# Performance work log

Measured on AMD Instinct MI355X. Metric: run time of the kernel, lower is better.

The kernel has to match this reference:

```python
import jax, jax.numpy as jnp
import numpy as np

B, S, D = 4, 2048, 1024

def setup_inputs() -> dict:
    key = jax.random.key(0)
    ks = jax.random.split(key, 7)
    sc = 1.0 / np.sqrt(D)
    return {
        "x": jax.random.normal(ks[0], (B, S, D), dtype=jnp.float32),
        "Wq": jax.random.normal(ks[1], (D, D), dtype=jnp.float32) * sc,
        "bq": jax.random.normal(ks[2], (D,), dtype=jnp.float32) * 0.01,
        "Wk": jax.random.normal(ks[3], (D, D), dtype=jnp.float32) * sc,
        "bk": jax.random.normal(ks[4], (D,), dtype=jnp.float32) * 0.01,
        "Wv": jax.random.normal(ks[5], (D, D), dtype=jnp.float32) * sc,
        "bv": jax.random.normal(ks[6], (D,), dtype=jnp.float32) * 0.01,
    }

def reference(x, Wq, bq, Wk, bk, Wv, bv):
    # q, k, v: [B, S, D] projections (torch Linear: x @ W^T + b; here W stored as [in, out])
    q = jnp.einsum("bsd,df->bsf", x, Wq) + bq
    k = jnp.einsum("bsd,df->bsf", x, Wk) + bk
    v = jnp.einsum("bsd,df->bsf", x, Wv) + bv
    dim = x.shape[-1]
    # scores: [B, S, S], scaled by sqrt(full d_model) as in the source
    scores = jnp.einsum("bqd,bkd->bqk", q, k) / jnp.sqrt(jnp.float32(dim)).astype(x.dtype)
    attn = jax.nn.softmax(scores, axis=-1)
    return jnp.einsum("bqk,bkd->bqd", attn, v)
```

## Files before the change

### kernel.cpp

```cpp
#include <hip/hip_runtime.h>
#include <hip/hip_bf16.h>

typedef __attribute__((ext_vector_type(8))) short bf16x8;
typedef __attribute__((ext_vector_type(4))) float f32x4;
typedef unsigned short u16;

__device__ __forceinline__ u16 f2bf(float f) {
  unsigned int u = __builtin_bit_cast(unsigned int, f);
  u += 0x7fffu + ((u >> 16) & 1u);
  return (u16)(u >> 16);
}
__device__ __forceinline__ float bf2f(unsigned int h) {
  unsigned int u = h << 16;
  return __builtin_bit_cast(float, u);
}

__device__ __forceinline__ void gload_lds16(const void* g, void* l) {
  __builtin_amdgcn_global_load_lds(
      (const __attribute__((address_space(1))) void*)g,
      (__attribute__((address_space(3))) void*)l, 16, 0, 0);
}

#define BAR() __builtin_amdgcn_s_barrier()
#define VMC(N) asm volatile("s_waitcnt vmcnt(%0)" ::"n"(N) : "memory")

template <int EPI>
__global__ __launch_bounds__(512, 2) void gemm8q(
    const u16* __restrict__ Abase, const u16* __restrict__ Btbase,
    const float* __restrict__ p0, float* __restrict__ p1,
    const float* __restrict__ p2, void* __restrict__ out0,
    void* __restrict__ out1, int Kd, int ldc, long long sAz, long long sBz,
    long long sCz) {
  constexpr int HSZ = 16384;
  constexpr int BUFSZ = 4 * HSZ;
  __shared__ char lds[2 * BUFSZ];

  const int gx = gridDim.x, gy = gridDim.y;
  const int nwg = gx * gy * gridDim.z;
  const int orig = blockIdx.x + gx * (blockIdx.y + gy * blockIdx.z);
  const int q = nwg >> 3, r = nwg & 7;
  const int xcd = orig & 7, loc = orig >> 3;
  const int wgid =
      (xcd < r ? xcd * (q + 1) : r * (q + 1) + (xcd - r) * q) + loc;
  const int bxi = wgid % gx;
  const int byi = (wgid / gx) % gy;
  const int z = wgid / (gx * gy);

  const int tid = threadIdx.x;
  const int w = tid >> 6, l = tid & 63;
  const int wr = w >> 2, wc = w & 3;
  const int lq = l >> 4, lr = l & 15;
  const int bm = byi * 256, bn = bxi * 256;
  const u16* A = Abase + (size_t)z * sAz;
  const u16* Bt = Btbase + (size_t)z * sBz;
  const int NT = Kd >> 6;

  const int kbp = ((tid & 7) ^ ((tid >> 3) & 7)) * 8;
  const int drow = tid >> 3;
  const u16* gA[2][2];
  const u16* gB[2][2];
#pragma unroll
  for (int h = 0; h < 2; ++h)
#pragma unroll
    for (int u = 0; u < 2; ++u) {
      gA[h][u] = A + (size_t)(bm + h * 128 + u * 64 + drow) * Kd + kbp;
      gB[h][u] = Bt + (size_t)(bn + h * 128 + u * 64 + drow) * Kd + kbp;
    }
  auto stageA = [&](int buf, int h, int kt) {
    char* d = lds + buf * BUFSZ + h * HSZ + tid * 16;
    gload_lds16(gA[h][0] + kt * 64, d);
    gload_lds16(gA[h][1] + kt * 64, d + 8192);
  };
  auto stageB = [&](int buf, int h, int kt) {
    char* d = lds + buf * BUFSZ + (2 + h) * HSZ + tid * 16;
    gload_lds16(gB[h][0] + kt * 64, d);
    gload_lds16(gB[h][1] + kt * 64, d + 8192);
  };

  const int ah = wr;
  const int bh = wc >> 1;
  const int bc0 = (wc & 1) * 64;
  const int sel = lr & 7;
  int koff[2];
#pragma unroll
  for (int kh = 0; kh < 2; ++kh) koff[kh] = (((kh * 4 + lq) ^ sel) << 4);

  f32x4 acc[8][4] = {};
  bf16x8 bb[4][2];
  bf16x8 a[2][2];

  stageA(0, 0, 0);
  stageA(0, 1, 0);
  stageB(0, 0, 0);
  stageB(0, 1, 0);
  stageA(1, 0, 1);
  stageA(1, 1, 1);
  stageB(1, 0, 1);
  stageB(1, 1, 1);
  VMC(8);
  BAR();

  for (int u = 0; u < NT; ++u) {
    const int buf = u & 1, obuf = buf ^ 1;
#pragma unroll
    for (int qp = 0; qp < 4; ++qp) {
      const char* pA = lds + buf * BUFSZ + ah * HSZ;
#pragma unroll
      for (int mf2 = 0; mf2 < 2; ++mf2)
#pragma unroll
        for (int kh = 0; kh < 2; ++kh)
          a[mf2][kh] = *(const bf16x8*)(pA + (qp * 32 + mf2 * 16 + lr) * 128 +
                                        koff[kh]);
      if (qp == 0) {
        const char* pB = lds + buf * BUFSZ + (2 + bh) * HSZ;
#pragma unroll
        for (int nf = 0; nf < 4; ++nf)
#pragma unroll
          for (int kh = 0; kh < 2; ++kh)
            bb[nf][kh] = *(const bf16x8*)(pB + (bc0 + nf * 16 + lr) * 128 +
                                          koff[kh]);
      }
      if (qp == 0 && u >= 1 && u + 1 < NT) stageA(obuf, 0, u + 1);
      if (qp == 1 && u >= 1 && u + 1 < NT) stageA(obuf, 1, u + 1);
      if (qp == 2 && u + 2 < NT) stageB(buf, 0, u + 2);
      if (qp == 3 && u + 2 < NT) stageB(buf, 1, u + 2);
      BAR();
      __builtin_amdgcn_s_setprio(1);
#pragma unroll
      for (int kh = 0; kh < 2; ++kh)
#pragma unroll
        for (int mf2 = 0; mf2 < 2; ++mf2)
#pragma unroll
          for (int nf = 0; nf < 4; ++nf)
            acc[qp * 2 + mf2][nf] = __builtin_amdgcn_mfma_f32_16x16x32_bf16(
                a[mf2][kh], bb[nf][kh], acc[qp * 2 + mf2][nf], 0, 0, 0);
      __builtin_amdgcn_s_setprio(0);
      if (qp == 3) {
        if (u + 2 < NT) {
          VMC(4);
        } else if (u + 1 < NT) {
          VMC(0);
        }
      }
      BAR();
    }
  }

  if constexpr (EPI == 4) {
    constexpr float K2 = 0.045084834f;
    u16* C = (u16*)out0 + (size_t)z * sCz;
    const float* cc = p0 + z * 2048;
    float* rs = p1 + z * 2048;
#pragma unroll
    for (int mf = 0; mf < 8; ++mf) {
      const int row = bm + wr * 128 + mf * 16 + lq * 4;
      float ps[4] = {0.f, 0.f, 0.f, 0.f};
#pragma unroll
      for (int nf = 0; nf < 4; ++nf) {
        const int col = bn + wc * 64 + nf * 16 + lr;
        const float cj2 = cc[col];
#pragma unroll
        for (int e = 0; e < 4; ++e) {
          const float pv = exp2f(fmaf(acc[mf][nf][e], K2, cj2));
          C[(size_t)(row + e) * ldc + col] = f2bf(pv);
          ps[e] += pv;
        }
      }
#pragma unroll
      for (int off = 1; off <= 8; off <<= 1)
#pragma unroll
        for (int e = 0; e < 4; ++e) ps[e] += __shfl_xor(ps[e], off, 64);
      if (lr == 0) {
#pragma unroll
        for (int e = 0; e < 4; ++e) atomicAdd(&rs[row + e], ps[e]);
      }
    }
  } else {
    const int mat = bn >> 10;
    u16* T = (u16*)out0;
    u16* V = (u16*)out1;
#pragma unroll
    for (int nf = 0; nf < 4; ++nf) {
      const int oc = (bn + wc * 64 + nf * 16 + lr) & 1023;
      if (mat == 0) {
#pragma unroll
        for (int mf = 0; mf < 8; ++mf) {
          const int row = bm + wr * 128 + mf * 16 + lq * 4;
#pragma unroll
          for (int e = 0; e < 4; ++e)
            T[(size_t)(row + e) * 1024 + oc] = f2bf(acc[mf][nf][e]);
        }
      } else {
        const float bb2 = p2[oc];
#pragma unroll
        for (int mf = 0; mf < 8; ++mf) {
          const int row = bm + wr * 128 + mf * 16 + lq * 4;
          const int bz = row >> 11, sdx = row & 2047;
          ushort4 pk;
          pk.x = f2bf(acc[mf][nf][0] + bb2);
          pk.y = f2bf(acc[mf][nf][1] + bb2);
          pk.z = f2bf(acc[mf][nf][2] + bb2);
          pk.w = f2bf(acc[mf][nf][3] + bb2);
          *(ushort4*)&V[((size_t)bz * 1024 + oc) * 2048 + sdx] = pk;
        }
      }
    }
  }
}

template <int EPI>
__global__ __launch_bounds__(512, 2) void gemm2t(
    const u16* __restrict__ Abase, const u16* __restrict__ Btbase,
    const float* __restrict__ p0, float* __restrict__ p1,
    const float* __restrict__ p2, void* __restrict__ out0,
    void* __restrict__ out1, int Kd, int ldc, long long sAz, long long sBz,
    long long sCz) {
  constexpr int ASZ = 16384;
  constexpr int BSZ = 32768;
  constexpr int BBASE = 2 * ASZ;
  __shared__ char lds[2 * ASZ + 3 * BSZ];

  const int gx = gridDim.x, gy = gridDim.y;
  const int nwg = gx * gy * gridDim.z;
  const int orig = blockIdx.x + gx * (blockIdx.y + gy * blockIdx.z);
  const int q = nwg >> 3, r = nwg & 7;
  const int xcd = orig & 7, loc = orig >> 3;
  const int wgid =
      (xcd < r ? xcd * (q + 1) : r * (q + 1) + (xcd - r) * q) + loc;
  const int bxi = wgid % gx;
  const int byi = (wgid / gx) % gy;
  const int z = wgid / (gx * gy);

  const int tid = threadIdx.x;
  const int w = tid >> 6, l = tid & 63;
  const int wr = w >> 2, wc = w & 3;
  const int lq = l >> 4, lr = l & 15;
  const int bm = byi * 128, bn = bxi * 256;
  const u16* A = Abase + (size_t)z * sAz;
  const u16* Bt = Btbase + (size_t)z * sBz;
  const int NT = Kd >> 6;

  const int kbp = ((tid & 7) ^ ((tid >> 3) & 7)) * 8;
  const int drow = tid >> 3;
  const u16* gA[2];
  const u16* gB[4];
#pragma unroll
  for (int u = 0; u < 2; ++u)
    gA[u] = A + (size_t)(bm + u * 64 + drow) * Kd + kbp;
#pragma unroll
  for (int u = 0; u < 4; ++u)
    gB[u] = Bt + (size_t)(bn + u * 64 + drow) * Kd + kbp;

  auto stageA = [&](int kt) {
    char* d = lds + (kt & 1) * ASZ + tid * 16;
#pragma unroll
    for (int u = 0; u < 2; ++u) gload_lds16(gA[u] + kt * 64, d + u * 8192);
  };
  auto stageB = [&](int kt) {
    char* d = lds + BBASE + (kt % 3) * BSZ + tid * 16;
#pragma unroll
    for (int u = 0; u < 4; ++u) gload_lds16(gB[u] + kt * 64, d + u * 8192);
  };

  const int rA = wr * 64 + lr;
  const int rB0 = wc * 64 + lr;
  int aoff[2];
#pragma unroll
  for (int kh = 0; kh < 2; ++kh)
    aoff[kh] = rA * 128 + (((kh * 4 + lq) ^ (rA & 7)) << 4);

  f32x4 acc[4][2][2] = {};
  bf16x8 a[2][4];
  bf16x8 bb[2][2][2];

  auto rdA = [&](int kt) {
    const char* p = lds + (kt & 1) * ASZ;
#pragma unroll
    for (int kh = 0; kh < 2; ++kh)
#pragma unroll
      for (int mf = 0; mf < 4; ++mf)
        a[kh][mf] = *(const bf16x8*)(p + aoff[kh] + mf * 2048);
  };
  auto rdB = [&](int kt) {
    const char* p = lds + BBASE + (kt % 3) * BSZ;
#pragma unroll
    for (int nh = 0; nh < 2; ++nh) {
      const int rB = rB0 + nh * 32;
#pragma unroll
      for (int kh = 0; kh < 2; ++kh) {
        const int o = rB * 128 + (((kh * 4 + lq) ^ (rB & 7)) << 4);
#pragma unroll
        for (int nf = 0; nf < 2; ++nf)
          bb[nh][kh][nf] = *(const bf16x8*)(p + o + nf * 2048);
      }
    }
  };
  auto mma = [&](int kh) {
    __builtin_amdgcn_s_setprio(1);
#pragma unroll
    for (int nh = 0; nh < 2; ++nh)
#pragma unroll
      for (int mf = 0; mf < 4; ++mf)
#pragma unroll
        for (int nf = 0; nf < 2; ++nf)
          acc[mf][nh][nf] = __builtin_amdgcn_mfma_f32_16x16x32_bf16(
              a[kh][mf], bb[nh][kh][nf], acc[mf][nh][nf], 0, 0, 0);
    __builtin_amdgcn_s_setprio(0);
  };

  stageB(0);
  stageA(0);
  stageB(1);
  stageA(1);
  VMC(6);
  BAR();

  for (int t = 0; t < NT; ++t) {
    rdA(t);
    rdB(t);
    if (t + 2 < NT) stageB(t + 2);
    BAR();
    mma(0);
    if (t + 2 < NT) VMC(4); else VMC(0);
    BAR();
    if (t + 2 < NT) stageA(t + 2);
    mma(1);
  }

  float* C = (float*)out0 + (size_t)z * sCz;
  const float* rs = p1 + z * 2048;
#pragma unroll
  for (int nh = 0; nh < 2; ++nh)
#pragma unroll
    for (int nf = 0; nf < 2; ++nf) {
      const int col = bn + wc * 64 + nh * 32 + nf * 16 + lr;
#pragma unroll
      for (int mf = 0; mf < 4; ++mf) {
        const int row = bm + wr * 64 + mf * 16 + lq * 4;
#pragma unroll
        for (int e = 0; e < 4; ++e)
          C[(size_t)(row + e) * ldc + col] = acc[mf][nh][nf][e] / rs[row + e];
      }
    }
}

__global__ __launch_bounds__(256) void gemmM(
    const u16* __restrict__ Abase, const u16* __restrict__ Btbase,
    float* __restrict__ out0, int Kd, int Kext, int ldc, long long sAz,
    long long sBz, long long sCz) {
  constexpr int ASZ = 16384;
  constexpr int BSZ = 16384;
  constexpr int BBASE = 2 * ASZ;
  __shared__ char lds[2 * ASZ + 3 * BSZ];

  const int tid = threadIdx.x;
  const int w = tid >> 6, l = tid & 63;
  const int wr = w >> 1, wc = w & 1;
  const int lq = l >> 4, lr = l & 15;
  const int bm = blockIdx.y * 128, bn = blockIdx.x * 128;
  const int z = blockIdx.z;
  const u16* A = Abase + (size_t)z * sAz;
  const u16* Bt = Btbase + (size_t)z * sBz;
  const int NT = Kext >> 6;

  const int kbp = ((tid & 7) ^ ((tid >> 3) & 7)) * 8;
  const int drow = tid >> 3;
  const u16* gA[4];
  const u16* gB[4];
#pragma unroll
  for (int u = 0; u < 4; ++u) {
    gA[u] = A + (size_t)(bm + u * 32 + drow) * Kd + kbp;
    gB[u] = Bt + (size_t)(bn + u * 32 + drow) * Kd + kbp;
  }

  auto stageA = [&](int kt) {
    char* d = lds + (kt & 1) * ASZ + tid * 16;
#pragma unroll
    for (int u = 0; u < 4; ++u) gload_lds16(gA[u] + kt * 64, d + u * 4096);
  };
  auto stageB = [&](int kt) {
    char* d = lds + BBASE + (kt % 3) * BSZ + tid * 16;
#pragma unroll
    for (int u = 0; u < 4; ++u) gload_lds16(gB[u] + kt * 64, d + u * 4096);
  };

  const int rA = wr * 64 + lr;
  const int rB0 = wc * 64 + lr;
  int aoff[2];
#pragma unroll
  for (int kh = 0; kh < 2; ++kh)
    aoff[kh] = rA * 128 + (((kh * 4 + lq) ^ (rA & 7)) << 4);

  f32x4 acc[4][2][2] = {};
  bf16x8 a[2][4];
  bf16x8 bb[2][2][2];

  auto rdA = [&](int kt) {
    const char* p = lds + (kt & 1) * ASZ;
#pragma unroll
    for (int kh = 0; kh < 2; ++kh)
#pragma unroll
      for (int mf = 0; mf < 4; ++mf)
        a[kh][mf] = *(const bf16x8*)(p + aoff[kh] + mf * 2048);
  };
  auto rdB = [&](int kt) {
    const char* p = lds + BBASE + (kt % 3) * BSZ;
#pragma unroll
    for (int nh = 0; nh < 2; ++nh) {
      const int rB = rB0 + nh * 32;
#pragma unroll
      for (int kh = 0; kh < 2; ++kh) {
        const int o = rB * 128 + (((kh * 4 + lq) ^ (rB & 7)) << 4);
#pragma unroll
        for (int nf = 0; nf < 2; ++nf)
          bb[nh][kh][nf] = *(const bf16x8*)(p + o + nf * 2048);
      }
    }
  };
  auto mma = [&](int kh) {
#pragma unroll
    for (int nh = 0; nh < 2; ++nh)
#pragma unroll
      for (int mf = 0; mf < 4; ++mf)
#pragma unroll
        for (int nf = 0; nf < 2; ++nf)
          acc[mf][nh][nf] = __builtin_amdgcn_mfma_f32_16x16x32_bf16(
              a[kh][mf], bb[nh][kh][nf], acc[mf][nh][nf], 0, 0, 0);
  };

  stageB(0);
  stageA(0);
  stageB(1);
  stageA(1);
  VMC(8);
  BAR();

  for (int t = 0; t < NT; ++t) {
    rdA(t);
    rdB(t);
    if (t + 2 < NT) stageB(t + 2);
    BAR();
    mma(0);
    if (t + 2 < NT) VMC(4); else VMC(0);
    BAR();
    if (t + 2 < NT) stageA(t + 2);
    mma(1);
  }

  float* C = out0 + (size_t)z * sCz;
#pragma unroll
  for (int nh = 0; nh < 2; ++nh)
#pragma unroll
    for (int nf = 0; nf < 2; ++nf) {
      const int col = bn + wc * 64 + nh * 32 + nf * 16 + lr;
#pragma unroll
      for (int mf = 0; mf < 4; ++mf) {
        const int row = bm + wr * 64 + mf * 16 + lq * 4;
#pragma unroll
        for (int e = 0; e < 4; ++e)
          C[(size_t)(row + e) * ldc + col] = acc[mf][nh][nf][e];
      }
    }
}

__global__ __launch_bounds__(256) void prep(
    const float* __restrict__ x, const float* __restrict__ Wq,
    const float* __restrict__ Wk, const float* __restrict__ Wv,
    const float* __restrict__ bq, u16* __restrict__ xb,
    u16* __restrict__ Wqb, u16* __restrict__ Wkb, u16* __restrict__ WtTV,
    float* __restrict__ vvec) {
  const int bid = blockIdx.x;
  const int tid = threadIdx.x;
  if (bid < 8192) {
    const int i = bid * 256 + tid;
    const float4 v = ((const float4*)x)[i];
    ushort4 o;
    o.x = f2bf(v.x);
    o.y = f2bf(v.y);
    o.z = f2bf(v.z);
    o.w = f2bf(v.w);
    ((ushort4*)xb)[i] = o;
  } else if (bid < 11264) {
    const int b = bid - 8192;
    const int zz = b >> 10, t2 = b & 1023;
    const int k0 = (t2 >> 5) * 32, n0 = (t2 & 31) * 32;
    const int tx = tid & 31, ty0 = tid >> 5;
    if (zz == 2) {
      __shared__ float s[32][33];
#pragma unroll
      for (int r = 0; r < 4; ++r) {
        const int row = ty0 + 8 * r;
        s[row][tx] = Wv[(size_t)(k0 + row) * 1024 + n0 + tx];
      }
      __syncthreads();
#pragma unroll
      for (int r = 0; r < 4; ++r) {
        const int row = ty0 + 8 * r;
        WtTV[1048576 + (size_t)(n0 + row) * 1024 + k0 + tx] =
            f2bf(s[tx][row]);
      }
    } else {
      const float* W = zz ? Wk : Wq;
      u16* O = zz ? Wkb : Wqb;
#pragma unroll
      for (int r = 0; r < 4; ++r) {
        const size_t i = (size_t)(k0 + ty0 + 8 * r) * 1024 + n0 + tx;
        O[i] = f2bf(W[i]);
      }
    }
  } else {
    const int d = bid - 11264;
    const float4 wv = ((const float4*)(Wk + (size_t)d * 1024))[tid];
    const float4 bv = ((const float4*)bq)[tid];
    float p = wv.x * bv.x + wv.y * bv.y + wv.z * bv.z + wv.w * bv.w;
#pragma unroll
    for (int o = 32; o; o >>= 1) p += __shfl_xor(p, o, 64);
    __shared__ float red[4];
    if ((tid & 63) == 0) red[tid >> 6] = p;
    __syncthreads();
    if (tid == 0) vvec[d] = red[0] + red[1] + red[2] + red[3];
  }
}

__global__ __launch_bounds__(256) void mck(const float* __restrict__ Mf,
                                           u16* __restrict__ Mt,
                                           const u16* __restrict__ xb,
                                           const float* __restrict__ v,
                                           float* __restrict__ c,
                                           float* __restrict__ rowsum) {
  const int bid = blockIdx.x;
  const int tid = threadIdx.x;
  if (bid < 1024) {
    const int i = bid * 256 + tid;
    const float4 a = ((const float4*)Mf)[i];
    const float4 b = ((const float4*)(Mf + 1048576))[i];
    const float4 cc = ((const float4*)(Mf + 2097152))[i];
    const float4 d = ((const float4*)(Mf + 3145728))[i];
    ushort4 o;
    o.x = f2bf(a.x + b.x + cc.x + d.x);
    o.y = f2bf(a.y + b.y + cc.y + d.y);
    o.z = f2bf(a.z + b.z + cc.z + d.z);
    o.w = f2bf(a.w + b.w + cc.w + d.w);
    ((ushort4*)Mt)[i] = o;
  } else {
    const int b2 = bid - 1024;
    if (b2 < 32) rowsum[b2 * 256 + tid] = 0.f;
    const int j = b2 * 8 + (tid >> 5);
    const int lane = tid & 31;
    const u16* xr = xb + (size_t)j * 1024;
    float p = 0.f;
#pragma unroll
    for (int k = 0; k < 4; ++k) {
      const int g = k * 32 + lane;
      const uint4 u = ((const uint4*)xr)[g];
      const float4 v0 = ((const float4*)v)[g * 2];
      const float4 v1 = ((const float4*)v)[g * 2 + 1];
      p += bf2f(u.x & 0xffffu) * v0.x + bf2f(u.x >> 16) * v0.y +
           bf2f(u.y & 0xffffu) * v0.z + bf2f(u.y >> 16) * v0.w +
           bf2f(u.z & 0xffffu) * v1.x + bf2f(u.z >> 16) * v1.y +
           bf2f(u.w & 0xffffu) * v1.z + bf2f(u.w >> 16) * v1.w;
    }
#pragma unroll
    for (int o = 16; o; o >>= 1) p += __shfl_xor(p, o, 64);
    if (lane == 0) c[j] = p * 0.045084834f;
  }
}

extern "C" void kernel_launch(void* const* d_in, const int* in_sizes, int n_in,
                              void* d_out, int out_size, void* d_ws,
                              size_t ws_size, hipStream_t stream) {
  const float* x = (const float*)d_in[0];
  const float* Wq = (const float*)d_in[1];
  const float* bq = (const float*)d_in[2];
  const float* Wk = (const float*)d_in[3];
  const float* Wv = (const float*)d_in[5];
  const float* bv = (const float*)d_in[6];
  float* out = (float*)d_out;
  char* ws = (char*)d_ws;

  u16* xb = (u16*)ws;
  u16* WtTV = (u16*)(ws + 16777216);
  u16* Wqb = (u16*)(ws + 20971520);
  u16* Wkb = (u16*)(ws + 23068672);
  float* vvec = (float*)(ws + 25165824);
  float* cvec = (float*)(ws + 25169920);
  float* rowsum = (float*)(ws + 25202688);
  float* Mf32 = (float*)(ws + 25235456);
  u16* T = (u16*)(ws + 25235456);
  u16* Vt = (u16*)(ws + 42012672);
  u16* SP = (u16*)(ws + 58789888);

  prep<<<12288, 256, 0, stream>>>(x, Wq, Wk, Wv, bq, xb, Wqb, Wkb, WtTV,
                                  vvec);

  gemmM<<<dim3(8, 8, 4), 256, 0, stream>>>(Wkb, Wqb, Mf32, 1024, 256, 1024,
                                           256LL, 256LL, 1048576LL);

  mck<<<2048, 256, 0, stream>>>(Mf32, WtTV, xb, vvec, cvec, rowsum);

  gemm8q<7><<<dim3(8, 32, 1), 512, 0, stream>>>(
      xb, WtTV, nullptr, nullptr, bv, T, Vt, 1024, 0, 0, 0, 0);

  gemm8q<4><<<dim3(8, 8, 4), 512, 0, stream>>>(
      T, xb, cvec, rowsum, nullptr, SP, nullptr, 1024, 2048, 2097152LL,
      2097152LL, 4194304LL);

  gemm2t<5><<<dim3(4, 16, 4), 512, 0, stream>>>(
      SP, Vt, nullptr, rowsum, nullptr, out, nullptr, 2048, 1024, 4194304LL,
      2097152LL, 2097152LL);
}
```

Before: 151.3 us.

## Restructure P·V GEMM into double-buffered half-tile pipeline with split quadrant compute

Replaces the P·V GEMM kernel with a version that double-buffers A and B together in one LDS buffer per stage instead of a 2-deep A ring and 3-deep B ring. The main loop splits each K-tile into two half-M passes, reading B fragments once and A fragments per pass, and interleaves global-to-LDS staging of the next tiles between the passes. The wave layout changes so each wave covers 64x64 with a 4x4 accumulator array. The aim is lower LDS footprint and better overlap of loads with MFMA, at the cost of extra barriers per tile.

```diff
diff --git a/kernel.cpp b/kernel.cpp
--- a/kernel.cpp
+++ b/kernel.cpp
@@ -208,17 +208,14 @@
   }
 }
 
-template <int EPI>
-__global__ __launch_bounds__(512, 2) void gemm2t(
+__global__ __launch_bounds__(512, 2) void gemm2q(
     const u16* __restrict__ Abase, const u16* __restrict__ Btbase,
-    const float* __restrict__ p0, float* __restrict__ p1,
-    const float* __restrict__ p2, void* __restrict__ out0,
-    void* __restrict__ out1, int Kd, int ldc, long long sAz, long long sBz,
-    long long sCz) {
-  constexpr int ASZ = 16384;
-  constexpr int BSZ = 32768;
-  constexpr int BBASE = 2 * ASZ;
-  __shared__ char lds[2 * ASZ + 3 * BSZ];
+    const float* __restrict__ rs_all, float* __restrict__ outp, int Kd,
+    int ldc, long long sAz, long long sBz, long long sCz) {
+  constexpr int AHSZ = 8192;
+  constexpr int BHSZ = 16384;
+  constexpr int BUFSZ = 2 * AHSZ + 2 * BHSZ;
+  __shared__ char lds[2 * BUFSZ];
 
   const int gx = gridDim.x, gy = gridDim.y;
   const int nwg = gx * gy * gridDim.z;
@@ -242,106 +239,107 @@
 
   const int kbp = ((tid & 7) ^ ((tid >> 3) & 7)) * 8;
   const int drow = tid >> 3;
-  const u16* gA[2];
-  const u16* gB[4];
-#pragma unroll
-  for (int u = 0; u < 2; ++u)
-    gA[u] = A + (size_t)(bm + u * 64 + drow) * Kd + kbp;
-#pragma unroll
-  for (int u = 0; u < 4; ++u)
-    gB[u] = Bt + (size_t)(bn + u * 64 + drow) * Kd + kbp;
-
-  auto stageA = [&](int kt) {
-    char* d = lds + (kt & 1) * ASZ + tid * 16;
-#pragma unroll
-    for (int u = 0; u < 2; ++u) gload_lds16(gA[u] + kt * 64, d + u * 8192);
-  };
-  auto stageB = [&](int kt) {
-    char* d = lds + BBASE + (kt % 3) * BSZ + tid * 16;
-#pragma unroll
-    for (int u = 0; u < 4; ++u) gload_lds16(gB[u] + kt * 64, d + u * 8192);
-  };
-
-  const int rA = wr * 64 + lr;
-  const int rB0 = wc * 64 + lr;
-  int aoff[2];
-#pragma unroll
-  for (int kh = 0; kh < 2; ++kh)
-    aoff[kh] = rA * 128 + (((kh * 4 + lq) ^ (rA & 7)) << 4);
-
-  f32x4 acc[4][2][2] = {};
-  bf16x8 a[2][4];
-  bf16x8 bb[2][2][2];
-
-  auto rdA = [&](int kt) {
-    const char* p = lds + (kt & 1) * ASZ;
-#pragma unroll
-    for (int kh = 0; kh < 2; ++kh)
-#pragma unroll
-      for (int mf = 0; mf < 4; ++mf)
-        a[kh][mf] = *(const bf16x8*)(p + aoff[kh] + mf * 2048);
-  };
-  auto rdB = [&](int kt) {
-    const char* p = lds + BBASE + (kt % 3) * BSZ;
-#pragma unroll
-    for (int nh = 0; nh < 2; ++nh) {
-      const int rB = rB0 + nh * 32;
-#pragma unroll
-      for (int kh = 0; kh < 2; ++kh) {
-        const int o = rB * 128 + (((kh * 4 + lq) ^ (rB & 7)) << 4);
-#pragma unroll
-        for (int nf = 0; nf < 2; ++nf)
-          bb[nh][kh][nf] = *(const bf16x8*)(p + o + nf * 2048);
-      }
-    }
-  };
-  auto mma = [&](int kh) {
-    __builtin_amdgcn_s_setprio(1);
-#pragma unroll
-    for (int nh = 0; nh < 2; ++nh)
-#pragma unroll
-      for (int mf = 0; mf < 4; ++mf)
-#pragma unroll
-        for (int nf = 0; nf < 2; ++nf)
-          acc[mf][nh][nf] = __builtin_amdgcn_mfma_f32_16x16x32_bf16(
-              a[kh][mf], bb[nh][kh][nf], acc[mf][nh][nf], 0, 0, 0);
-    __builtin_amdgcn_s_setprio(0);
-  };
-
-  stageB(0);
-  stageA(0);
-  stageB(1);
-  stageA(1);
+  const u16* gAq[2];
+  const u16* gB[2][2];
+#pragma unroll
+  for (int h = 0; h < 2; ++h) {
+    gAq[h] = A + (size_t)(bm + h * 64 + drow) * Kd + kbp;
+#pragma unroll
+    for (int u = 0; u < 2; ++u)
+      gB[h][u] = Bt + (size_t)(bn + h * 128 + u * 64 + drow) * Kd + kbp;
+  }
+  auto stageA = [&](int buf, int kt) {
+    char* d = lds + buf * BUFSZ + tid * 16;
+    gload_lds16(gAq[0] + kt * 64, d);
+    gload_lds16(gAq[1] + kt * 64, d + AHSZ);
+  };
+  auto stageB = [&](int buf, int h, int kt) {
+    char* d = lds + buf * BUFSZ + 2 * AHSZ + h * BHSZ + tid * 16;
+    gload_lds16(gB[h][0] + kt * 64, d);
+    gload_lds16(gB[h][1] + kt * 64, d + 8192);
+  };
+
+  const int ah = wr;
+  const int bh = wc >> 1;
+  const int bc0 = (wc & 1) * 64;
+  const int sel = lr & 7;
+  int koff[2];
+#pragma unroll
+  for (int kh = 0; kh < 2; ++kh) koff[kh] = (((kh * 4 + lq) ^ sel) << 4);
+
+  f32x4 acc[4][4] = {};
+  bf16x8 bb[4][2];
+  bf16x8 a[2][2];
+
+  stageA(0, 0);
+  stageB(0, 0, 0);
+  stageB(0, 1, 0);
+  stageA(1, 1);
+  stageB(1, 0, 1);
+  stageB(1, 1, 1);
   VMC(6);
   BAR();
 
-  for (int t = 0; t < NT; ++t) {
-    rdA(t);
-    rdB(t);
-    if (t + 2 < NT) stageB(t + 2);
-    BAR();
-    mma(0);
-    if (t + 2 < NT) VMC(4); else VMC(0);
-    BAR();
-    if (t + 2 < NT) stageA(t + 2);
-    mma(1);
-  }
-
-  float* C = (float*)out0 + (size_t)z * sCz;
-  const float* rs = p1 + z * 2048;
-#pragma unroll
-  for (int nh = 0; nh < 2; ++nh)
-#pragma unroll
-    for (int nf = 0; nf < 2; ++nf) {
-      const int col = bn + wc * 64 + nh * 32 + nf * 16 + lr;
-#pragma unroll
-      for (int mf = 0; mf < 4; ++mf) {
-        const int row = bm + wr * 64 + mf * 16 + lq * 4;
-#pragma unroll
-        for (int e = 0; e < 4; ++e)
-          C[(size_t)(row + e) * ldc + col] = acc[mf][nh][nf][e] / rs[row + e];
-      }
-    }
+  for (int u = 0; u < NT; ++u) {
+    const int buf = u & 1, obuf = buf ^ 1;
+#pragma unroll
+    for (int qp = 0; qp < 2; ++qp) {
+      const char* pA = lds + buf * BUFSZ + ah * AHSZ;
+#pragma unroll
+      for (int mf2 = 0; mf2 < 2; ++mf2)
+#pragma unroll
+        for (int kh = 0; kh < 2; ++kh)
+          a[mf2][kh] = *(const bf16x8*)(pA + (qp * 32 + mf2 * 16 + lr) * 128 +
+                                        koff[kh]);
+      if (qp == 0) {
+        const char* pB = lds + buf * BUFSZ + 2 * AHSZ + bh * BHSZ;
+#pragma unroll
+        for (int nf = 0; nf < 4; ++nf)
+#pragma unroll
+          for (int kh = 0; kh < 2; ++kh)
+            bb[nf][kh] = *(const bf16x8*)(pB + (bc0 + nf * 16 + lr) * 128 +
+                                          koff[kh]);
+      }
+      if (qp == 0 && u >= 1 && u + 1 < NT) stageA(obuf, u + 1);
+      if (qp == 1 && u + 2 < NT) {
+        stageB(buf, 0, u + 2);
+        stageB(buf, 1, u + 2);
+      }
+      BAR();
+      __builtin_amdgcn_s_setprio(1);
+#pragma unroll
+      for (int kh = 0; kh < 2; ++kh)
+#pragma unroll
+        for (int mf2 = 0; mf2 < 2; ++mf2)
+#pragma unroll
+          for (int nf = 0; nf < 4; ++nf)
+            acc[qp * 2 + mf2][nf] = __builtin_amdgcn_mfma_f32_16x16x32_bf16(
+                a[mf2][kh], bb[nf][kh], acc[qp * 2 + mf2][nf], 0, 0, 0);
+      __builtin_amdgcn_s_setprio(0);
+      if (qp == 1) {
+        if (u + 2 < NT) {
+          VMC(4);
+        } else if (u + 1 < NT) {
+          VMC(0);
+        }
+      }
+      BAR();
+    }
+  }
+
+  float* C = outp + (size_t)z * sCz;
+  const float* rs = rs_all + z * 2048;
+#pragma unroll
+  for (int mf = 0; mf < 4; ++mf) {
+    const int row = bm + wr * 64 + (mf >> 1) * 32 + (mf & 1) * 16 + lq * 4;
+#pragma unroll
+    for (int nf = 0; nf < 4; ++nf) {
+      const int col = bn + wc * 64 + nf * 16 + lr;
+#pragma unroll
+      for (int e = 0; e < 4; ++e)
+        C[(size_t)(row + e) * ldc + col] = acc[mf][nf][e] / rs[row + e];
+    }
+  }
 }
 
 __global__ __launch_bounds__(256) void gemmM(
@@ -605,7 +603,6 @@
       T, xb, cvec, rowsum, nullptr, SP, nullptr, 1024, 2048, 2097152LL,
       2097152LL, 4194304LL);
 
-  gemm2t<5><<<dim3(4, 16, 4), 512, 0, stream>>>(
-      SP, Vt, nullptr, rowsum, nullptr, out, nullptr, 2048, 1024, 4194304LL,
-      2097152LL, 2097152LL);
-}
+  gemm2q<<<dim3(4, 16, 4), 512, 0, stream>>>(SP, Vt, rowsum, out, 2048, 1024,
+                                             4194304LL, 2097152LL, 2097152LL);
+}
```

Result: no change. 153.3 us (+1.4%).
